# Performance work log

Hardware: AMD Instinct MI355X
Metric: run time of the kernel (lower is better)

## Reference

```python
import jax, jax.numpy as jnp
import numpy as np

NUM_HEADS = 8
EPS = 1e-12  # torch F.normalize default eps


def _l2_normalize(t, axis):
    n = jnp.sqrt(jnp.sum(t * t, axis=axis, keepdims=True))
    return t / jnp.maximum(n, EPS)


def setup_inputs() -> dict:
    key = jax.random.key(0)
    k1, k2, k3 = jax.random.split(key, 3)
    B, N, D = 32, 3136, 384
    x = jax.random.normal(k1, (B, N, D), dtype=jnp.float32)
    qkv_w = jax.random.normal(k2, (3 * D, D), dtype=jnp.float32) * (1.0 / np.sqrt(D))
    temperature = jnp.ones((NUM_HEADS, 1, 1), dtype=jnp.float32)
    proj_w = jax.random.normal(k3, (D, D), dtype=jnp.float32) * (1.0 / np.sqrt(D))
    proj_b = jnp.zeros((D,), dtype=jnp.float32)
    return {"x": x, "qkv_w": qkv_w, "temperature": temperature,
            "proj_w": proj_w, "proj_b": proj_b}


def reference(x, qkv_w, temperature, proj_w, proj_b):
    B, N, D = x.shape
    H = NUM_HEADS
    C = D // H
    # qkv projection (no bias), split last dim as (3, H, C) -> (3, B, H, C, N)
    qkv = jnp.einsum('bnd,ed->bne', x, qkv_w)
    qkv = qkv.reshape(B, N, 3, H, C).transpose(2, 0, 3, 4, 1)
    q, k, v = qkv[0], qkv[1], qkv[2]            # each (B, H, C, N)
    q = _l2_normalize(q, axis=-1)               # normalize over tokens N
    k = _l2_normalize(k, axis=-1)
    # cross-covariance attention: (B, H, C, C), scaled by per-head temperature
    attn = jnp.einsum('bhcn,bhdn->bhcd', q, k) * temperature
    attn = jax.nn.softmax(attn, axis=-1)
    out = jnp.einsum('bhcd,bhdn->bhcn', attn, v)  # (B, H, C, N)
    out = out.transpose(0, 3, 1, 2).reshape(B, N, D)
    return jnp.einsum('bnd,ed->bne', out, proj_w) + proj_b
```

## Files before the change

### kernel.cpp

```cpp
#include <hip/hip_runtime.h>


typedef __bf16 bf16x8 __attribute__((ext_vector_type(8)));
typedef float floatx4 __attribute__((ext_vector_type(4)));
typedef unsigned short u16;

#define B_ 32
#define N_ 3136
#define D_ 384
#define H_ 8
#define C_ 48
#define BN_ 100352

__device__ __forceinline__ u16 f2b(float f) {
  unsigned u = __builtin_bit_cast(unsigned, f);
  u += 0x7FFFu + ((u >> 16) & 1u);
  return (u16)(u >> 16);
}
__device__ __forceinline__ void gload16(const u16* g, u16* l) {
  __builtin_amdgcn_global_load_lds(
      (const __attribute__((address_space(1))) void*)g,
      (__attribute__((address_space(3))) void*)l, 16, 0, 0);
}

__global__ __launch_bounds__(256) void k_cvt(const float* __restrict__ in,
                                             u16* __restrict__ out, int n4) {
  int i = blockIdx.x * 256 + threadIdx.x;
  if (i < n4) {
    float4 v = ((const float4*)in)[i];
    ushort4 o;
    o.x = f2b(v.x); o.y = f2b(v.y); o.z = f2b(v.z); o.w = f2b(v.w);
    ((ushort4*)out)[i] = o;
  }
}

__global__ __launch_bounds__(256) void k_cvt_t(const float* __restrict__ x,
                                               u16* __restrict__ xbf,
                                               u16* __restrict__ xT) {
  int d0 = blockIdx.x * 64, n0 = blockIdx.y * 64, b = blockIdx.z;
  const float* xp = x + ((size_t)b * N_ + n0) * D_ + d0;
  __shared__ u16 L[64][68];
  int t = threadIdx.x;
  int nl = t >> 4, dl = (t & 15) * 4;
#pragma unroll
  for (int p = 0; p < 4; p++) {
    int n = nl + p * 16;
    float4 v = *(const float4*)(xp + (size_t)n * D_ + dl);
    ushort4 o;
    o.x = f2b(v.x); o.y = f2b(v.y); o.z = f2b(v.z); o.w = f2b(v.w);
    *(ushort4*)(xbf + ((size_t)(b * N_ + n0 + n)) * D_ + d0 + dl) = o;
    *(ushort4*)(&L[n][dl]) = o;
  }
  __syncthreads();
  int dl2 = t >> 4, nl2 = (t & 15) * 4;
#pragma unroll
  for (int p = 0; p < 4; p++) {
    int d = dl2 + p * 16;
    ushort4 o;
    o.x = L[nl2 + 0][d]; o.y = L[nl2 + 1][d];
    o.z = L[nl2 + 2][d]; o.w = L[nl2 + 3][d];
    *(ushort4*)(xT + (size_t)(d0 + d) * BN_ + b * N_ + n0 + nl2) = o;
  }
}

__global__ __launch_bounds__(256) void k_wvt(const float* __restrict__ qkv_w,
                                             u16* __restrict__ wvT) {
  int h = blockIdx.x, t = threadIdx.x;
  for (int idx = t; idx < 384 * 64; idx += 256) {
    int j = idx >> 6, d = idx & 63;
    float v = (d < 48) ? qkv_w[(size_t)(2 * D_ + h * C_ + d) * D_ + j] : 0.f;
    wvT[(size_t)h * 24576 + idx] = f2b(v);
  }
}

__global__ __launch_bounds__(256) void k_gram(const u16* __restrict__ xT,
                                              float* __restrict__ G) {
  int tile = blockIdx.x, b = blockIdx.y, ns = blockIdx.z * 448;
  int m0 = (tile % 3) * 128, n0 = (tile / 3) * 128;
  __shared__ u16 As[2][128][32];
  __shared__ u16 Bs[2][128][32];
  int t = threadIdx.x, wid = t >> 6, lane = t & 63;
  int srow = wid * 32 + (lane >> 2), scol = (lane & 3) * 8;
  int wm = (wid & 1) * 64, wn = (wid >> 1) * 64;
  int r = lane & 15, quad = lane >> 4, q8 = quad * 8;
  const u16* base = xT + (size_t)b * N_ + ns + scol;
  const u16* gA = base + (size_t)(m0 + srow) * BN_;
  const u16* gB = base + (size_t)(n0 + srow) * BN_;

  floatx4 acc[4][4] = {};
  for (int k0 = 0; k0 < 448; k0 += 64) {
#pragma unroll
    for (int ks = 0; ks < 2; ks++) {
      gload16(gA + k0 + ks * 32,                     &As[ks][wid * 32][0]);
      gload16(gA + k0 + ks * 32 + (size_t)16 * BN_,  &As[ks][wid * 32 + 16][0]);
      gload16(gB + k0 + ks * 32,                     &Bs[ks][wid * 32][0]);
      gload16(gB + k0 + ks * 32 + (size_t)16 * BN_,  &Bs[ks][wid * 32 + 16][0]);
    }
    __syncthreads();
#pragma unroll
    for (int ks = 0; ks < 2; ks++) {
      bf16x8 af[4], bf[4];
#pragma unroll
      for (int i = 0; i < 4; i++) af[i] = *(const bf16x8*)(&As[ks][wm + i * 16 + r][q8]);
#pragma unroll
      for (int j = 0; j < 4; j++) bf[j] = *(const bf16x8*)(&Bs[ks][wn + j * 16 + r][q8]);
#pragma unroll
      for (int i = 0; i < 4; i++)
#pragma unroll
        for (int j = 0; j < 4; j++)
          acc[i][j] = __builtin_amdgcn_mfma_f32_16x16x32_bf16(af[i], bf[j], acc[i][j], 0, 0, 0);
    }
    __syncthreads();
  }
  float* Gb = G + (size_t)b * 147456;
#pragma unroll
  for (int i = 0; i < 4; i++)
#pragma unroll
    for (int j = 0; j < 4; j++)
#pragma unroll
      for (int v = 0; v < 4; v++) {
        int rr = m0 + wm + i * 16 + quad * 4 + v;
        int cc = n0 + wn + j * 16 + r;
        atomicAdd(&Gb[(size_t)rr * 384 + cc], acc[i][j][v]);
      }
}

__global__ __launch_bounds__(256) void k_mid1(const u16* __restrict__ wbf,
                                              const u16* __restrict__ Gb,
                                              float* __restrict__ U) {
  int m0 = blockIdx.x * 128, n0 = blockIdx.y * 128, b = blockIdx.z;
  __shared__ u16 As[2][128][32];
  __shared__ u16 Bs[2][128][32];
  int t = threadIdx.x, wid = t >> 6, lane = t & 63;
  int srow = wid * 32 + (lane >> 2), scol = (lane & 3) * 8;
  int wm = (wid & 1) * 64, wn = (wid >> 1) * 64;
  int r = lane & 15, quad = lane >> 4, q8 = quad * 8;
  const u16* gA = wbf + (size_t)(m0 + srow) * 384 + scol;
  const u16* gB = Gb + (size_t)b * 147456 + (size_t)(n0 + srow) * 384 + scol;

  floatx4 acc[4][4] = {};
  for (int k0 = 0; k0 < 384; k0 += 64) {
#pragma unroll
    for (int ks = 0; ks < 2; ks++) {
      gload16(gA + k0 + ks * 32,            &As[ks][wid * 32][0]);
      gload16(gA + k0 + ks * 32 + 16 * 384, &As[ks][wid * 32 + 16][0]);
      gload16(gB + k0 + ks * 32,            &Bs[ks][wid * 32][0]);
      gload16(gB + k0 + ks * 32 + 16 * 384, &Bs[ks][wid * 32 + 16][0]);
    }
    __syncthreads();
#pragma unroll
    for (int ks = 0; ks < 2; ks++) {
      bf16x8 af[4], bf[4];
#pragma unroll
      for (int i = 0; i < 4; i++) af[i] = *(const bf16x8*)(&As[ks][wm + i * 16 + r][q8]);
#pragma unroll
      for (int j = 0; j < 4; j++) bf[j] = *(const bf16x8*)(&Bs[ks][wn + j * 16 + r][q8]);
#pragma unroll
      for (int i = 0; i < 4; i++)
#pragma unroll
        for (int j = 0; j < 4; j++)
          acc[i][j] = __builtin_amdgcn_mfma_f32_16x16x32_bf16(af[i], bf[j], acc[i][j], 0, 0, 0);
    }
    __syncthreads();
  }
  float* Ub = U + (size_t)b * 294912;
#pragma unroll
  for (int i = 0; i < 4; i++)
#pragma unroll
    for (int j = 0; j < 4; j++)
#pragma unroll
      for (int v = 0; v < 4; v++) {
        int rr = m0 + wm + i * 16 + quad * 4 + v;
        int cc = n0 + wn + j * 16 + r;
        Ub[(size_t)rr * 384 + cc] = acc[i][j][v];
      }
}

__global__ __launch_bounds__(256) void k_mid2(const float* __restrict__ U,
                                              const u16* __restrict__ wbf,
                                              const u16* __restrict__ wvT,
                                              const float* __restrict__ temp,
                                              u16* __restrict__ MT) {
  int bh = blockIdx.x, b = bh >> 3, h = bh & 7;
  __shared__ __align__(16) u16 sUq[48][32], sUk[48][32], sWq[48][32], sWk[48][32];
  __shared__ __align__(16) u16 sA[48][72];
  __shared__ float sSsq[96];
  __shared__ float sInv[96];
  int t = threadIdx.x, wid = t >> 6, lane = t & 63;
  int r = lane & 15, quad = lane >> 4, q8 = quad * 8;
  const float* Uq = U + (size_t)b * 294912 + (size_t)(h * C_) * 384;
  const float* Uk = U + (size_t)b * 294912 + (size_t)(D_ + h * C_) * 384;
  const u16* Wq = wbf + (size_t)(h * C_) * 384;
  const u16* Wk = wbf + (size_t)(D_ + h * C_) * 384;

  floatx4 accS[3] = {};
  floatx4 accD[6] = {};
  for (int k0 = 0; k0 < 384; k0 += 32) {
    for (int idx = t; idx < 768; idx += 256) {
      int tile = idx / 192, rem = idx - tile * 192;
      int rr = rem >> 2, c8 = (rem & 3) * 8;
      if (tile < 2) {
        const float* src = (tile == 0 ? Uq : Uk) + (size_t)rr * 384 + k0 + c8;
        float4 a = *(const float4*)src;
        float4 bb = *(const float4*)(src + 4);
        ushort4 lo, hi;
        lo.x = f2b(a.x); lo.y = f2b(a.y); lo.z = f2b(a.z); lo.w = f2b(a.w);
        hi.x = f2b(bb.x); hi.y = f2b(bb.y); hi.z = f2b(bb.z); hi.w = f2b(bb.w);
        u16* dst = (tile == 0 ? &sUq[rr][c8] : &sUk[rr][c8]);
        *(ushort4*)dst = lo;
        *(ushort4*)(dst + 4) = hi;
      } else {
        const u16* src = (tile == 2 ? Wq : Wk) + (size_t)rr * 384 + k0 + c8;
        u16* dst = (tile == 2 ? &sWq[rr][c8] : &sWk[rr][c8]);
        *(int4*)dst = *(const int4*)src;
      }
    }
    __syncthreads();
    if (wid < 3) {
      bf16x8 uq = *(const bf16x8*)(&sUq[wid * 16 + r][q8]);
#pragma unroll
      for (int j = 0; j < 3; j++) {
        bf16x8 wk = *(const bf16x8*)(&sWk[j * 16 + r][q8]);
        accS[j] = __builtin_amdgcn_mfma_f32_16x16x32_bf16(uq, wk, accS[j], 0, 0, 0);
      }
    } else {
#pragma unroll
      for (int i = 0; i < 3; i++) {
        bf16x8 uq = *(const bf16x8*)(&sUq[i * 16 + r][q8]);
        bf16x8 wq = *(const bf16x8*)(&sWq[i * 16 + r][q8]);
        bf16x8 uk = *(const bf16x8*)(&sUk[i * 16 + r][q8]);
        bf16x8 wk = *(const bf16x8*)(&sWk[i * 16 + r][q8]);
        accD[i]     = __builtin_amdgcn_mfma_f32_16x16x32_bf16(uq, wq, accD[i], 0, 0, 0);
        accD[3 + i] = __builtin_amdgcn_mfma_f32_16x16x32_bf16(uk, wk, accD[3 + i], 0, 0, 0);
      }
    }
    __syncthreads();
  }
  if (wid == 3) {
#pragma unroll
    for (int i = 0; i < 3; i++)
#pragma unroll
      for (int v = 0; v < 4; v++)
        if (r == quad * 4 + v) {
          sSsq[i * 16 + r] = accD[i][v];
          sSsq[48 + i * 16 + r] = accD[3 + i][v];
        }
  }
  __syncthreads();
  if (t < 96) sInv[t] = 1.f / fmaxf(sqrtf(sSsq[t]), 1e-12f);
  __syncthreads();
  for (int idx = t; idx < 48 * 16; idx += 256) sA[idx >> 4][48 + (idx & 15)] = 0;
  float T = temp[h];
  if (wid < 3) {
    float L[3][4];
    int c_base = wid * 16 + quad * 4;
#pragma unroll
    for (int j = 0; j < 3; j++)
#pragma unroll
      for (int v = 0; v < 4; v++)
        L[j][v] = accS[j][v] * sInv[c_base + v] * sInv[48 + j * 16 + r] * T;
    float mx[4], sum[4];
#pragma unroll
    for (int v = 0; v < 4; v++) mx[v] = fmaxf(fmaxf(L[0][v], L[1][v]), L[2][v]);
#pragma unroll
    for (int m = 1; m <= 8; m <<= 1)
#pragma unroll
      for (int v = 0; v < 4; v++) mx[v] = fmaxf(mx[v], __shfl_xor(mx[v], m));
#pragma unroll
    for (int v = 0; v < 4; v++) sum[v] = 0.f;
#pragma unroll
    for (int j = 0; j < 3; j++)
#pragma unroll
      for (int v = 0; v < 4; v++) { L[j][v] = __expf(L[j][v] - mx[v]); sum[v] += L[j][v]; }
#pragma unroll
    for (int m = 1; m <= 8; m <<= 1)
#pragma unroll
      for (int v = 0; v < 4; v++) sum[v] += __shfl_xor(sum[v], m);
#pragma unroll
    for (int j = 0; j < 3; j++)
#pragma unroll
      for (int v = 0; v < 4; v++)
        sA[c_base + v][j * 16 + r] = f2b(L[j][v] / sum[v]);
  }
  __syncthreads();
  const u16* WvTh = wvT + (size_t)h * 24576;
  floatx4 accM[3][6] = {};
#pragma unroll
  for (int ks = 0; ks < 2; ks++) {
    bf16x8 af[3];
#pragma unroll
    for (int i = 0; i < 3; i++) af[i] = *(const bf16x8*)(&sA[i * 16 + r][ks * 32 + q8]);
#pragma unroll
    for (int jj = 0; jj < 6; jj++) {
      int j = wid * 96 + jj * 16 + r;
      bf16x8 bb = *(const bf16x8*)(WvTh + (size_t)j * 64 + ks * 32 + q8);
#pragma unroll
      for (int i = 0; i < 3; i++)
        accM[i][jj] = __builtin_amdgcn_mfma_f32_16x16x32_bf16(af[i], bb, accM[i][jj], 0, 0, 0);
    }
  }
  u16* MTb = MT + (size_t)b * 147456;
#pragma unroll
  for (int i = 0; i < 3; i++)
#pragma unroll
    for (int jj = 0; jj < 6; jj++)
#pragma unroll
      for (int v = 0; v < 4; v++) {
        int c = i * 16 + quad * 4 + v;
        int j = wid * 96 + jj * 16 + r;
        MTb[(size_t)j * 384 + h * C_ + c] = f2b(accM[i][jj][v]);
      }
}

__global__ __launch_bounds__(256) void k_mid3(const u16* __restrict__ pwbf,
                                              const u16* __restrict__ MT,
                                              u16* __restrict__ R) {
  int m0 = (blockIdx.x % 3) * 128, n0 = (blockIdx.x / 3) * 128, b = blockIdx.y;
  __shared__ u16 As[2][128][32];
  __shared__ u16 Bs[2][128][32];
  int t = threadIdx.x, wid = t >> 6, lane = t & 63;
  int srow = wid * 32 + (lane >> 2), scol = (lane & 3) * 8;
  int wm = (wid & 1) * 64, wn = (wid >> 1) * 64;
  int r = lane & 15, quad = lane >> 4, q8 = quad * 8;
  const u16* gA = pwbf + (size_t)(m0 + srow) * 384 + scol;
  const u16* gB = MT + (size_t)b * 147456 + (size_t)(n0 + srow) * 384 + scol;

  floatx4 acc[4][4] = {};
  for (int k0 = 0; k0 < 384; k0 += 64) {
#pragma unroll
    for (int ks = 0; ks < 2; ks++) {
      gload16(gA + k0 + ks * 32,            &As[ks][wid * 32][0]);
      gload16(gA + k0 + ks * 32 + 16 * 384, &As[ks][wid * 32 + 16][0]);
      gload16(gB + k0 + ks * 32,            &Bs[ks][wid * 32][0]);
      gload16(gB + k0 + ks * 32 + 16 * 384, &Bs[ks][wid * 32 + 16][0]);
    }
    __syncthreads();
#pragma unroll
    for (int ks = 0; ks < 2; ks++) {
      bf16x8 af[4], bf[4];
#pragma unroll
      for (int i = 0; i < 4; i++) af[i] = *(const bf16x8*)(&As[ks][wm + i * 16 + r][q8]);
#pragma unroll
      for (int j = 0; j < 4; j++) bf[j] = *(const bf16x8*)(&Bs[ks][wn + j * 16 + r][q8]);
#pragma unroll
      for (int i = 0; i < 4; i++)
#pragma unroll
        for (int j = 0; j < 4; j++)
          acc[i][j] = __builtin_amdgcn_mfma_f32_16x16x32_bf16(af[i], bf[j], acc[i][j], 0, 0, 0);
    }
    __syncthreads();
  }
  u16* Rb = R + (size_t)b * 147456;
#pragma unroll
  for (int i = 0; i < 4; i++)
#pragma unroll
    for (int j = 0; j < 4; j++)
#pragma unroll
      for (int v = 0; v < 4; v++) {
        int rr = m0 + wm + i * 16 + quad * 4 + v;
        int cc = n0 + wn + j * 16 + r;
        Rb[(size_t)rr * 384 + cc] = f2b(acc[i][j][v]);
      }
}

__global__ __launch_bounds__(256) void k_final(const u16* __restrict__ xbf,
                                               const u16* __restrict__ R,
                                               const float* __restrict__ bias,
                                               float* __restrict__ Y) {
  int lin = blockIdx.y * 3 + blockIdx.x;
  int w = (lin & 7) * 588 + (lin >> 3);
  int ft = w % 3, gt = w / 3;
  int b = gt / 49, n0 = (gt % 49) * 64;
  size_t g0 = (size_t)b * N_ + n0;
  int f0 = ft * 128;
  __shared__ u16 As[2][64][32];
  __shared__ u16 Bs[2][128][32];
  int t = threadIdx.x, wid = t >> 6, lane = t & 63;
  int srow = t >> 2, scol = (t & 3) * 8;
  int wm = (wid & 1) * 32, wn = (wid >> 1) * 64;
  int r = lane & 15, quad = lane >> 4, q8 = quad * 8;
  const u16* gA = xbf + (g0 + srow) * 384 + scol;
  const u16* gB1 = R + (size_t)b * 147456 + (size_t)(f0 + srow) * 384 + scol;
  const u16* gB2 = gB1 + (size_t)64 * 384;

  floatx4 acc[2][4] = {};
  for (int k0 = 0; k0 < 384; k0 += 64) {
#pragma unroll
    for (int ks = 0; ks < 2; ks++) {
      gload16(gA + k0 + ks * 32,  &As[ks][wid * 16][0]);
      gload16(gB1 + k0 + ks * 32, &Bs[ks][wid * 16][0]);
      gload16(gB2 + k0 + ks * 32, &Bs[ks][64 + wid * 16][0]);
    }
    __syncthreads();
#pragma unroll
    for (int ks = 0; ks < 2; ks++) {
      bf16x8 af[2], bf[4];
#pragma unroll
      for (int i = 0; i < 2; i++) af[i] = *(const bf16x8*)(&As[ks][wm + i * 16 + r][q8]);
#pragma unroll
      for (int j = 0; j < 4; j++) bf[j] = *(const bf16x8*)(&Bs[ks][wn + j * 16 + r][q8]);
#pragma unroll
      for (int i = 0; i < 2; i++)
#pragma unroll
        for (int j = 0; j < 4; j++)
          acc[i][j] = __builtin_amdgcn_mfma_f32_16x16x32_bf16(af[i], bf[j], acc[i][j], 0, 0, 0);
    }
    __syncthreads();
  }
#pragma unroll
  for (int i = 0; i < 2; i++)
#pragma unroll
    for (int j = 0; j < 4; j++) {
      int cc = wn + j * 16 + r;
      float bv = bias[f0 + cc];
#pragma unroll
      for (int v = 0; v < 4; v++) {
        int rr = wm + i * 16 + quad * 4 + v;
        Y[(g0 + rr) * 384 + f0 + cc] = acc[i][j][v] + bv;
      }
    }
}

extern "C" void kernel_launch(void* const* d_in, const int* in_sizes, int n_in,
                              void* d_out, int out_size, void* d_ws, size_t ws_size,
                              hipStream_t stream) {
  const float* x      = (const float*)d_in[0];
  const float* qkv_w  = (const float*)d_in[1];
  const float* temp   = (const float*)d_in[2];
  const float* proj_w = (const float*)d_in[3];
  const float* proj_b = (const float*)d_in[4];
  float* out = (float*)d_out;

  char* ws = (char*)d_ws;
  u16*   xbf  = (u16*)(ws);
  u16*   xT   = (u16*)(ws + 77070336);
  u16*   wbf  = (u16*)(ws + 154140672);
  u16*   pwbf = (u16*)(ws + 155025408);
  u16*   wvT  = (u16*)(ws + 155320320);
  float* G    = (float*)(ws + 155713536);
  u16*   Gbf  = (u16*)(ws + 174587904);
  float* U    = (float*)(ws + 184025088);
  u16*   MT   = (u16*)(ws + 221773824);
  u16*   R    = (u16*)(ws + 231211008);

  hipMemsetAsync(G, 0, 18874368, stream);

  k_cvt_t<<<dim3(6, 49, 32), 256, 0, stream>>>(x, xbf, xT);
  k_cvt<<<432, 256, 0, stream>>>(qkv_w, wbf, 110592);
  k_cvt<<<144, 256, 0, stream>>>(proj_w, pwbf, 36864);
  k_wvt<<<8, 256, 0, stream>>>(qkv_w, wvT);

  k_gram<<<dim3(9, 32, 7), 256, 0, stream>>>(xT, G);
  k_cvt<<<4608, 256, 0, stream>>>(G, Gbf, 1179648);
  k_mid1<<<dim3(6, 3, 32), 256, 0, stream>>>(wbf, Gbf, U);
  k_mid2<<<256, 256, 0, stream>>>(U, wbf, wvT, temp, MT);
  k_mid3<<<dim3(9, 32), 256, 0, stream>>>(pwbf, MT, R);
  k_final<<<dim3(3, 1568), 256, 0, stream>>>(xbf, R, proj_b, out);
}
```

Before: 557.6 us.

## Replace atomic split-K Gram with two-way split plus sum pass, remap blocks for XCD locality

The Gram kernel now splits the token dimension two ways instead of seven, so each block does a longer K loop. It writes plain stores into two partial buffers instead of using atomicAdd, which removes the memset and the atomic traffic; a new k_gsum kernel adds the partials and converts to bf16. The k_gram and k_mid1 grids are flattened and remapped so consecutive blocks of one batch land on the same XCD, which should improve L2 reuse. The three small weight-prep launches are merged into one kernel. In exchange the Gram launch has fewer blocks (576), which could lower occupancy, and the workspace grows.

```diff
diff --git a/kernel.cpp b/kernel.cpp
--- a/kernel.cpp
+++ b/kernel.cpp
@@ -21,17 +21,6 @@
   __builtin_amdgcn_global_load_lds(
       (const __attribute__((address_space(1))) void*)g,
       (__attribute__((address_space(3))) void*)l, 16, 0, 0);
-}
-
-__global__ __launch_bounds__(256) void k_cvt(const float* __restrict__ in,
-                                             u16* __restrict__ out, int n4) {
-  int i = blockIdx.x * 256 + threadIdx.x;
-  if (i < n4) {
-    float4 v = ((const float4*)in)[i];
-    ushort4 o;
-    o.x = f2b(v.x); o.y = f2b(v.y); o.z = f2b(v.z); o.w = f2b(v.w);
-    ((ushort4*)out)[i] = o;
-  }
 }
 
 __global__ __launch_bounds__(256) void k_cvt_t(const float* __restrict__ x,
@@ -63,32 +52,54 @@
   }
 }
 
-__global__ __launch_bounds__(256) void k_wvt(const float* __restrict__ qkv_w,
-                                             u16* __restrict__ wvT) {
-  int h = blockIdx.x, t = threadIdx.x;
-  for (int idx = t; idx < 384 * 64; idx += 256) {
-    int j = idx >> 6, d = idx & 63;
-    float v = (d < 48) ? qkv_w[(size_t)(2 * D_ + h * C_ + d) * D_ + j] : 0.f;
-    wvT[(size_t)h * 24576 + idx] = f2b(v);
+__global__ __launch_bounds__(256) void k_prep(const float* __restrict__ qkv_w,
+                                              const float* __restrict__ proj_w,
+                                              u16* __restrict__ wbf,
+                                              u16* __restrict__ pwbf,
+                                              u16* __restrict__ wvT) {
+  int blk = blockIdx.x, t = threadIdx.x;
+  if (blk < 432) {
+    int i = blk * 256 + t;
+    float4 v = ((const float4*)qkv_w)[i];
+    ushort4 o;
+    o.x = f2b(v.x); o.y = f2b(v.y); o.z = f2b(v.z); o.w = f2b(v.w);
+    ((ushort4*)wbf)[i] = o;
+  } else if (blk < 576) {
+    int i = (blk - 432) * 256 + t;
+    float4 v = ((const float4*)proj_w)[i];
+    ushort4 o;
+    o.x = f2b(v.x); o.y = f2b(v.y); o.z = f2b(v.z); o.w = f2b(v.w);
+    ((ushort4*)pwbf)[i] = o;
+  } else {
+    int h = blk - 576;
+    for (int idx = t; idx < 384 * 64; idx += 256) {
+      int j = idx >> 6, d = idx & 63;
+      float v = (d < 48) ? qkv_w[(size_t)(2 * D_ + h * C_ + d) * D_ + j] : 0.f;
+      wvT[(size_t)h * 24576 + idx] = f2b(v);
+    }
   }
 }
 
 __global__ __launch_bounds__(256) void k_gram(const u16* __restrict__ xT,
                                               float* __restrict__ G) {
-  int tile = blockIdx.x, b = blockIdx.y, ns = blockIdx.z * 448;
+  int lin = blockIdx.x;
+  int w = (lin & 7) * 72 + (lin >> 3);
+  int b = w / 18, rem = w % 18;
+  int split = rem / 9, tile = rem % 9;
   int m0 = (tile % 3) * 128, n0 = (tile / 3) * 128;
+  int kbeg = split * 1600, klen = split ? 1536 : 1600;
   __shared__ u16 As[2][128][32];
   __shared__ u16 Bs[2][128][32];
   int t = threadIdx.x, wid = t >> 6, lane = t & 63;
   int srow = wid * 32 + (lane >> 2), scol = (lane & 3) * 8;
   int wm = (wid & 1) * 64, wn = (wid >> 1) * 64;
   int r = lane & 15, quad = lane >> 4, q8 = quad * 8;
-  const u16* base = xT + (size_t)b * N_ + ns + scol;
+  const u16* base = xT + (size_t)b * N_ + kbeg + scol;
   const u16* gA = base + (size_t)(m0 + srow) * BN_;
   const u16* gB = base + (size_t)(n0 + srow) * BN_;
 
   floatx4 acc[4][4] = {};
-  for (int k0 = 0; k0 < 448; k0 += 64) {
+  for (int k0 = 0; k0 < klen; k0 += 64) {
 #pragma unroll
     for (int ks = 0; ks < 2; ks++) {
       gload16(gA + k0 + ks * 32,                     &As[ks][wid * 32][0]);
@@ -112,7 +123,7 @@
     }
     __syncthreads();
   }
-  float* Gb = G + (size_t)b * 147456;
+  float* Gp = G + (size_t)split * 4718592 + (size_t)b * 147456;
 #pragma unroll
   for (int i = 0; i < 4; i++)
 #pragma unroll
@@ -121,14 +132,28 @@
       for (int v = 0; v < 4; v++) {
         int rr = m0 + wm + i * 16 + quad * 4 + v;
         int cc = n0 + wn + j * 16 + r;
-        atomicAdd(&Gb[(size_t)rr * 384 + cc], acc[i][j][v]);
-      }
+        Gp[(size_t)rr * 384 + cc] = acc[i][j][v];
+      }
+}
+
+__global__ __launch_bounds__(256) void k_gsum(const float* __restrict__ G,
+                                              u16* __restrict__ Gbf) {
+  int i = blockIdx.x * 256 + threadIdx.x;
+  float4 a = ((const float4*)G)[i];
+  float4 b = ((const float4*)(G + 4718592))[i];
+  ushort4 o;
+  o.x = f2b(a.x + b.x); o.y = f2b(a.y + b.y);
+  o.z = f2b(a.z + b.z); o.w = f2b(a.w + b.w);
+  ((ushort4*)Gbf)[i] = o;
 }
 
 __global__ __launch_bounds__(256) void k_mid1(const u16* __restrict__ wbf,
                                               const u16* __restrict__ Gb,
                                               float* __restrict__ U) {
-  int m0 = blockIdx.x * 128, n0 = blockIdx.y * 128, b = blockIdx.z;
+  int lin = blockIdx.x;
+  int w = (lin & 7) * 72 + (lin >> 3);
+  int b = w / 18, rem = w % 18;
+  int m0 = (rem / 3) * 128, n0 = (rem % 3) * 128;
   __shared__ u16 As[2][128][32];
   __shared__ u16 Bs[2][128][32];
   int t = threadIdx.x, wid = t >> 6, lane = t & 63;
@@ -438,21 +463,17 @@
   u16*   pwbf = (u16*)(ws + 155025408);
   u16*   wvT  = (u16*)(ws + 155320320);
   float* G    = (float*)(ws + 155713536);
-  u16*   Gbf  = (u16*)(ws + 174587904);
-  float* U    = (float*)(ws + 184025088);
-  u16*   MT   = (u16*)(ws + 221773824);
-  u16*   R    = (u16*)(ws + 231211008);
-
-  hipMemsetAsync(G, 0, 18874368, stream);
+  u16*   Gbf  = (u16*)(ws + 193462272);
+  float* U    = (float*)(ws + 202899456);
+  u16*   MT   = (u16*)(ws + 240648192);
+  u16*   R    = (u16*)(ws + 250085376);
 
   k_cvt_t<<<dim3(6, 49, 32), 256, 0, stream>>>(x, xbf, xT);
-  k_cvt<<<432, 256, 0, stream>>>(qkv_w, wbf, 110592);
-  k_cvt<<<144, 256, 0, stream>>>(proj_w, pwbf, 36864);
-  k_wvt<<<8, 256, 0, stream>>>(qkv_w, wvT);
-
-  k_gram<<<dim3(9, 32, 7), 256, 0, stream>>>(xT, G);
-  k_cvt<<<4608, 256, 0, stream>>>(G, Gbf, 1179648);
-  k_mid1<<<dim3(6, 3, 32), 256, 0, stream>>>(wbf, Gbf, U);
+  k_prep<<<584, 256, 0, stream>>>(qkv_w, proj_w, wbf, pwbf, wvT);
+
+  k_gram<<<576, 256, 0, stream>>>(xT, G);
+  k_gsum<<<4608, 256, 0, stream>>>(G, Gbf);
+  k_mid1<<<576, 256, 0, stream>>>(wbf, Gbf, U);
   k_mid2<<<256, 256, 0, stream>>>(U, wbf, wvT, temp, MT);
   k_mid3<<<dim3(9, 32), 256, 0, stream>>>(pwbf, MT, R);
   k_final<<<dim3(3, 1568), 256, 0, stream>>>(xbf, R, proj_b, out);
```

Measured after the change: 494.5 us. -11.3%, faster.
